# Performance work log

Measured on AMD Instinct MI355X. Metric: run time of the kernel, lower is better.

The kernel has to match this reference:

```python
import jax, jax.numpy as jnp
import numpy as np

T = 8          # temporal window (hardcoded '8' in the original)
N = 2048       # num_neurons
S = 8192       # num_synapses per neuron
MAXW = 8.0
UCAPTURE = 10.0 / 128.0
UMINUS = 10.0 / 128.0
USEARCH = 1.0 / 128.0
UBACKOFF = 96.0 / 128.0
UMIN = 4.0 / 128.0


def setup_inputs() -> dict:
    key = jax.random.key(0)
    k1, k2, k3 = jax.random.split(key, 3)
    all_input_spikes = jax.random.randint(k1, (T, N, S), 0, 2, dtype=jnp.int32)
    all_output_spikes = jax.random.randint(k2, (T, N), 0, 2, dtype=jnp.int32)
    W = jax.random.uniform(k3, (N, S), dtype=jnp.float32, minval=-0.5, maxval=8.5)
    return {"all_input_spikes": all_input_spikes,
            "all_output_spikes": all_output_spikes,
            "W": W}


def reference(all_input_spikes, all_output_spikes, W):
    # Clamp weights to [0, 8] (the two torch.where clamps).
    w = jnp.clip(W, 0.0, MAXW)  # [N, S]

    # Spike times encoded as 8 - (spike count over the temporal window).
    in_t = (8 - jnp.sum(all_input_spikes, axis=0)).astype(jnp.int32)        # [N, S]
    out_t = (8 - jnp.sum(all_output_spikes, axis=0)).astype(jnp.int32)[:, None]  # [N, 1]

    wn = w / MAXW
    p_plus = wn * (2.0 - wn)            # Bernoulli prob for fplus
    p_minus = (1.0 - wn) * (1.0 + wn)   # Bernoulli prob for fminus

    rk = jax.random.split(jax.random.key(42), 8)
    dt = w.dtype
    fplus = jax.random.bernoulli(rk[0], p_plus).astype(dt)
    fminus = jax.random.bernoulli(rk[1], p_minus).astype(dt)
    ucap = jax.random.bernoulli(rk[2], UCAPTURE, (N, S)).astype(dt)
    uminus = jax.random.bernoulli(rk[3], UMINUS, (N, S)).astype(dt)
    usearch = jax.random.bernoulli(rk[4], USEARCH, (N, S)).astype(dt)
    ubackoff = jax.random.bernoulli(rk[5], UBACKOFF, (N, S)).astype(dt)
    # umin is sampled independently in each of the four branches
    umin1 = jax.random.bernoulli(rk[6], UMIN, (N, S)).astype(dt)
    k7a, k7b, k7c = jax.random.split(rk[7], 3)
    umin2 = jax.random.bernoulli(k7a, UMIN, (N, S)).astype(dt)
    umin3 = jax.random.bernoulli(k7b, UMIN, (N, S)).astype(dt)
    umin4 = jax.random.bernoulli(k7c, UMIN, (N, S)).astype(dt)

    in_fired = in_t < 8
    out_fired = out_t < 8

    # Branch 1: capture (input at or before output)
    b1 = jnp.where(in_fired & out_fired & (in_t <= out_t),
                   w + ucap * jnp.maximum(fplus, umin1), w)
    # Branch 2: minus (input after output)
    b2 = jnp.where(in_fired & out_fired & (in_t > out_t),
                   b1 - uminus * jnp.maximum(fminus, umin2), b1)
    # Branch 3: search (input fired, output silent)
    b3 = jnp.where(in_fired & (out_t == 8),
                   b2 + usearch * jnp.maximum(fplus, umin3), b2)
    # Branch 4: backoff (input silent, output fired)
    b4 = jnp.where((in_t == 8) & out_fired,
                   b3 - ubackoff * jnp.maximum(fminus, umin4), b3)
    return b4
```

## Files before the change

kernel.cpp:

```cpp
#include <hip/hip_runtime.h>

#define TT 8
#define NN 2048
#define SS 8192
#define MM (NN * SS)

#define TH_CAP10  655360u
#define TH_SEARCH 65536u
#define TH_BACK   6291456u
#define TH_MIN    262144u

#define NBLOCKS   2048
#define NTHREADS  (NBLOCKS * 256)
#define ITERS     (MM / 4 / NTHREADS)

typedef int   __attribute__((ext_vector_type(4))) intx4;
typedef float __attribute__((ext_vector_type(4))) floatx4;
typedef unsigned __attribute__((ext_vector_type(4))) uintx4;

struct Tbl { unsigned v[32]; };

__host__ __device__ __forceinline__ void tf2x32(unsigned k0, unsigned k1,
                                                unsigned x0, unsigned x1,
                                                unsigned& o0, unsigned& o1) {
  const unsigned ks2 = k0 ^ k1 ^ 0x1BD11BDAu;
  x0 += k0; x1 += k1;
#define TFR(r) { x0 += x1; x1 = (x1 << (r)) | (x1 >> (32 - (r))); x1 ^= x0; }
  TFR(13) TFR(15) TFR(26) TFR(6)
  x0 += k1;  x1 += ks2 + 1u;
  TFR(17) TFR(29) TFR(16) TFR(24)
  x0 += ks2; x1 += k0 + 2u;
  TFR(13) TFR(15) TFR(26) TFR(6)
  x0 += k0;  x1 += k1 + 3u;
  TFR(17) TFR(29) TFR(16) TFR(24)
  x0 += k1;  x1 += ks2 + 4u;
  TFR(13) TFR(15) TFR(26) TFR(6)
  x0 += ks2; x1 += k0 + 5u;
#undef TFR
  o0 = x0; o1 = x1;
}

__global__ __launch_bounds__(256) void ModSTDP_ocnt_kernel(
    const int* __restrict__ outS, int* __restrict__ ocnt) {
  const int n = blockIdx.x * blockDim.x + threadIdx.x;
  int s = 0;
#pragma unroll
  for (int t = 0; t < TT; ++t) s += outS[t * NN + n];
  ocnt[n] = s;
}

__device__ __forceinline__ void load_tile(const int* __restrict__ inS,
                                          const int* __restrict__ ocnt,
                                          const float* __restrict__ W,
                                          unsigned base,
                                          intx4 (&s)[TT], floatx4& w, int& o) {
#pragma unroll
  for (int t = 0; t < TT; ++t)
    s[t] = __builtin_nontemporal_load(
        reinterpret_cast<const intx4*>(inS + (size_t)t * MM + base));
  w = __builtin_nontemporal_load(reinterpret_cast<const floatx4*>(W + base));
  o = ocnt[base >> 13];
}

__device__ __forceinline__ void compute_tile(float* __restrict__ out,
                                             const unsigned* __restrict__ tbl,
                                             unsigned base,
                                             const intx4 (&s)[TT],
                                             const floatx4& w4, int o) {
  int cnt[4] = {0, 0, 0, 0};
#pragma unroll
  for (int t = 0; t < TT; ++t) {
    cnt[0] += s[t].x; cnt[1] += s[t].y; cnt[2] += s[t].z; cnt[3] += s[t].w;
  }
  const float wv[4] = {w4.x, w4.y, w4.z, w4.w};
  const bool outF = o > 0;
  float res[4];
#pragma unroll
  for (int e = 0; e < 4; ++e) {
    const unsigned j = base + (unsigned)e;
    const float w = fminf(fmaxf(wv[e], 0.0f), 8.0f);
    const int c = cnt[e];
    const bool inF = c > 0;
    const bool active = inF | outF;
    const unsigned idx = inF ? (outF ? ((c >= o) ? 0u : 1u) : 2u) : 3u;

    const uintx4 r0 = *reinterpret_cast<const uintx4*>(tbl + (idx << 3));
    const uintx4 r1 = *reinterpret_cast<const uintx4*>(tbl + (idx << 3) + 4);
    const unsigned ka0 = r0.x, ka1 = r0.y, kb0 = r0.z, kb1 = r0.w;
    const unsigned kc0 = r1.x, kc1 = r1.y, thB = r1.z;
    const float sgn = __uint_as_float(r1.w);

    const float wn = w * 0.125f;
    const float pp = __fmul_rn(wn, __fsub_rn(2.0f, wn));
    const float pm = __fmul_rn(__fsub_rn(1.0f, wn), __fadd_rn(1.0f, wn));
    const float pA = (idx & 1u) ? pm : pp;

    unsigned a0, a1, b0, b1, c0, c1;
    tf2x32(ka0, ka1, 0u, j, a0, a1);
    const unsigned bitsA = a0 ^ a1;
    const float u = __uint_as_float((bitsA >> 9) | 0x3f800000u) - 1.0f;
    const bool fab = u < pA;

    tf2x32(kb0, kb1, 0u, j, b0, b1);
    const bool gate = (((b0 ^ b1) >> 9) < thB);

    tf2x32(kc0, kc1, 0u, j, c0, c1);
    const bool um = (((c0 ^ c1) >> 9) < TH_MIN);

    const bool doit = active & gate & (fab | um);
    res[e] = doit ? __fadd_rn(w, sgn) : w;
  }
  floatx4 r;
  r.x = res[0]; r.y = res[1]; r.z = res[2]; r.w = res[3];
  __builtin_nontemporal_store(r, reinterpret_cast<floatx4*>(out + base));
}

__global__ __launch_bounds__(256) void ModSTDP_58823872086838_kernel(
    const int* __restrict__ inS,
    const int* __restrict__ ocnt,
    const float* __restrict__ W,
    float* __restrict__ out,
    Tbl tb)
{
  __shared__ __align__(16) unsigned tbl[32];
  if (threadIdx.x < 32) tbl[threadIdx.x] = tb.v[threadIdx.x];
  __syncthreads();

  const unsigned tid = blockIdx.x * blockDim.x + threadIdx.x;
  const unsigned STRIDE = (unsigned)NTHREADS << 2;

  intx4 sA[TT], sB[TT];
  floatx4 wA, wB;
  int oA, oB;

  unsigned base = tid << 2;
  load_tile(inS, ocnt, W, base, sA, wA, oA);

#pragma unroll 1
  for (int i = 0; i < ITERS; i += 2) {
    load_tile(inS, ocnt, W, base + STRIDE, sB, wB, oB);
    compute_tile(out, tbl, base, sA, wA, oA);
    if (i + 2 < ITERS)
      load_tile(inS, ocnt, W, base + 2 * STRIDE, sA, wA, oA);
    compute_tile(out, tbl, base + STRIDE, sB, wB, oB);
    base += 2 * STRIDE;
  }
}

extern "C" void kernel_launch(void* const* d_in, const int* in_sizes, int n_in,
                              void* d_out, int out_size, void* d_ws, size_t ws_size,
                              hipStream_t stream) {
  const int*   inS  = (const int*)d_in[0];
  const int*   outS = (const int*)d_in[1];
  const float* W    = (const float*)d_in[2];
  float*       out  = (float*)d_out;
  int*         ocnt = (int*)d_ws;

  unsigned kp[20];
  {
    unsigned rk[16];
    for (unsigned i = 0; i < 8; ++i) {
      unsigned o0, o1;
      tf2x32(0u, 42u, 0u, i, o0, o1);
      rk[2 * i] = o0; rk[2 * i + 1] = o1;
    }
    for (int i = 0; i < 14; ++i) kp[i] = rk[i];
    for (unsigned i = 0; i < 3; ++i) {
      unsigned o0, o1;
      tf2x32(rk[14], rk[15], 0u, i, o0, o1);
      kp[14 + 2 * i] = o0; kp[15 + 2 * i] = o1;
    }
  }

  Tbl tb;
  unsigned* v = tb.v;
  v[0] = kp[0];  v[1] = kp[1];  v[2] = kp[4];   v[3] = kp[5];
  v[4] = kp[12]; v[5] = kp[13]; v[6] = TH_CAP10; v[7] = 0x3f800000u;
  v[8] = kp[2];  v[9] = kp[3];  v[10] = kp[6];  v[11] = kp[7];
  v[12] = kp[14]; v[13] = kp[15]; v[14] = TH_CAP10; v[15] = 0xbf800000u;
  v[16] = kp[0]; v[17] = kp[1]; v[18] = kp[8];  v[19] = kp[9];
  v[20] = kp[16]; v[21] = kp[17]; v[22] = TH_SEARCH; v[23] = 0x3f800000u;
  v[24] = kp[2]; v[25] = kp[3]; v[26] = kp[10]; v[27] = kp[11];
  v[28] = kp[18]; v[29] = kp[19]; v[30] = TH_BACK; v[31] = 0xbf800000u;

  ModSTDP_ocnt_kernel<<<dim3(NN / 256), dim3(256), 0, stream>>>(outS, ocnt);
  ModSTDP_58823872086838_kernel<<<dim3(NBLOCKS), dim3(256), 0, stream>>>(
      inS, ocnt, W, out, tb);
}
```

Before: 136.4 us.

## Fuse output-count kernel and switch to one-shot 8-elements-per-thread grid

Removes the separate output-spike-count kernel and recomputes each neuron's output count inline from the 8 time steps. Replaces the persistent grid-stride loop with manual double-buffered prefetch with a large grid where each thread handles 8 contiguous elements in a single pass, and drops nontemporal hints on the loads. This saves a launch and the ocnt round trip but depends on hardware occupancy to hide latency instead of explicit prefetch, and it adds redundant small outS loads per thread.

```diff
diff --git a/kernel.cpp b/kernel.cpp
--- a/kernel.cpp
+++ b/kernel.cpp
@@ -10,9 +10,8 @@
 #define TH_BACK   6291456u
 #define TH_MIN    262144u
 
-#define NBLOCKS   2048
-#define NTHREADS  (NBLOCKS * 256)
-#define ITERS     (MM / 4 / NTHREADS)
+#define EPT       8
+#define NBLOCKS   (MM / 256 / EPT)
 
 typedef int   __attribute__((ext_vector_type(4))) intx4;
 typedef float __attribute__((ext_vector_type(4))) floatx4;
@@ -40,49 +39,53 @@
   o0 = x0; o1 = x1;
 }
 
-__global__ __launch_bounds__(256) void ModSTDP_ocnt_kernel(
-    const int* __restrict__ outS, int* __restrict__ ocnt) {
-  const int n = blockIdx.x * blockDim.x + threadIdx.x;
-  int s = 0;
+__global__ __launch_bounds__(256) void ModSTDP_58823872086838_kernel(
+    const int* __restrict__ inS,
+    const int* __restrict__ outS,
+    const float* __restrict__ W,
+    float* __restrict__ out,
+    Tbl tb)
+{
+  __shared__ __align__(16) unsigned tbl[32];
+  if (threadIdx.x < 32) tbl[threadIdx.x] = tb.v[threadIdx.x];
+  __syncthreads();
+
+  const unsigned tid  = blockIdx.x * blockDim.x + threadIdx.x;
+  const unsigned base = tid * EPT;
+  const unsigned n    = base >> 13;
+
+  int osum = 0;
 #pragma unroll
-  for (int t = 0; t < TT; ++t) s += outS[t * NN + n];
-  ocnt[n] = s;
-}
+  for (int t = 0; t < TT; ++t) osum += outS[t * NN + n];
+  const bool outF = osum > 0;
 
-__device__ __forceinline__ void load_tile(const int* __restrict__ inS,
-                                          const int* __restrict__ ocnt,
-                                          const float* __restrict__ W,
-                                          unsigned base,
-                                          intx4 (&s)[TT], floatx4& w, int& o) {
-#pragma unroll
-  for (int t = 0; t < TT; ++t)
-    s[t] = __builtin_nontemporal_load(
-        reinterpret_cast<const intx4*>(inS + (size_t)t * MM + base));
-  w = __builtin_nontemporal_load(reinterpret_cast<const floatx4*>(W + base));
-  o = ocnt[base >> 13];
-}
-
-__device__ __forceinline__ void compute_tile(float* __restrict__ out,
-                                             const unsigned* __restrict__ tbl,
-                                             unsigned base,
-                                             const intx4 (&s)[TT],
-                                             const floatx4& w4, int o) {
-  int cnt[4] = {0, 0, 0, 0};
+  intx4 s[TT][2];
 #pragma unroll
   for (int t = 0; t < TT; ++t) {
-    cnt[0] += s[t].x; cnt[1] += s[t].y; cnt[2] += s[t].z; cnt[3] += s[t].w;
+    const int* p = inS + (size_t)t * MM + base;
+    s[t][0] = *reinterpret_cast<const intx4*>(p);
+    s[t][1] = *reinterpret_cast<const intx4*>(p + 4);
   }
-  const float wv[4] = {w4.x, w4.y, w4.z, w4.w};
-  const bool outF = o > 0;
-  float res[4];
+  const floatx4 w0 = *reinterpret_cast<const floatx4*>(W + base);
+  const floatx4 w1 = *reinterpret_cast<const floatx4*>(W + base + 4);
+
+  int cnt[EPT] = {0, 0, 0, 0, 0, 0, 0, 0};
 #pragma unroll
-  for (int e = 0; e < 4; ++e) {
+  for (int t = 0; t < TT; ++t) {
+#pragma unroll
+    for (int e = 0; e < EPT; ++e) cnt[e] += s[t][e >> 2][e & 3];
+  }
+
+  float res[EPT];
+#pragma unroll
+  for (int e = 0; e < EPT; ++e) {
     const unsigned j = base + (unsigned)e;
-    const float w = fminf(fmaxf(wv[e], 0.0f), 8.0f);
+    const float wraw = (e < 4) ? w0[e & 3] : w1[e & 3];
+    const float w = fminf(fmaxf(wraw, 0.0f), 8.0f);
     const int c = cnt[e];
     const bool inF = c > 0;
     const bool active = inF | outF;
-    const unsigned idx = inF ? (outF ? ((c >= o) ? 0u : 1u) : 2u) : 3u;
+    const unsigned idx = inF ? (outF ? ((c >= osum) ? 0u : 1u) : 2u) : 3u;
 
     const uintx4 r0 = *reinterpret_cast<const uintx4*>(tbl + (idx << 3));
     const uintx4 r1 = *reinterpret_cast<const uintx4*>(tbl + (idx << 3) + 4);
@@ -110,41 +113,12 @@
     const bool doit = active & gate & (fab | um);
     res[e] = doit ? __fadd_rn(w, sgn) : w;
   }
-  floatx4 r;
-  r.x = res[0]; r.y = res[1]; r.z = res[2]; r.w = res[3];
-  __builtin_nontemporal_store(r, reinterpret_cast<floatx4*>(out + base));
-}
 
-__global__ __launch_bounds__(256) void ModSTDP_58823872086838_kernel(
-    const int* __restrict__ inS,
-    const int* __restrict__ ocnt,
-    const float* __restrict__ W,
-    float* __restrict__ out,
-    Tbl tb)
-{
-  __shared__ __align__(16) unsigned tbl[32];
-  if (threadIdx.x < 32) tbl[threadIdx.x] = tb.v[threadIdx.x];
-  __syncthreads();
-
-  const unsigned tid = blockIdx.x * blockDim.x + threadIdx.x;
-  const unsigned STRIDE = (unsigned)NTHREADS << 2;
-
-  intx4 sA[TT], sB[TT];
-  floatx4 wA, wB;
-  int oA, oB;
-
-  unsigned base = tid << 2;
-  load_tile(inS, ocnt, W, base, sA, wA, oA);
-
-#pragma unroll 1
-  for (int i = 0; i < ITERS; i += 2) {
-    load_tile(inS, ocnt, W, base + STRIDE, sB, wB, oB);
-    compute_tile(out, tbl, base, sA, wA, oA);
-    if (i + 2 < ITERS)
-      load_tile(inS, ocnt, W, base + 2 * STRIDE, sA, wA, oA);
-    compute_tile(out, tbl, base + STRIDE, sB, wB, oB);
-    base += 2 * STRIDE;
-  }
+  floatx4 r0, r1;
+  r0.x = res[0]; r0.y = res[1]; r0.z = res[2]; r0.w = res[3];
+  r1.x = res[4]; r1.y = res[5]; r1.z = res[6]; r1.w = res[7];
+  __builtin_nontemporal_store(r0, reinterpret_cast<floatx4*>(out + base));
+  __builtin_nontemporal_store(r1, reinterpret_cast<floatx4*>(out + base + 4));
 }
 
 extern "C" void kernel_launch(void* const* d_in, const int* in_sizes, int n_in,
@@ -154,7 +128,6 @@
   const int*   outS = (const int*)d_in[1];
   const float* W    = (const float*)d_in[2];
   float*       out  = (float*)d_out;
-  int*         ocnt = (int*)d_ws;
 
   unsigned kp[20];
   {
@@ -183,7 +156,6 @@
   v[24] = kp[2]; v[25] = kp[3]; v[26] = kp[10]; v[27] = kp[11];
   v[28] = kp[18]; v[29] = kp[19]; v[30] = TH_BACK; v[31] = 0xbf800000u;
 
-  ModSTDP_ocnt_kernel<<<dim3(NN / 256), dim3(256), 0, stream>>>(outS, ocnt);
   ModSTDP_58823872086838_kernel<<<dim3(NBLOCKS), dim3(256), 0, stream>>>(
-      inS, ocnt, W, out, tb);
+      inS, outS, W, out, tb);
 }
```

Measured after the change: 135.2 us. No clear change (-0.9%).
